# Performance work log

Measured on AMD Instinct MI355X. Metric: run time of the kernel, lower is better.

## Reference

```python
import jax, jax.numpy as jnp
import numpy as np

S, B, D, H, O = 128, 16, 512, 512, 256  # seq_len, batch, input=hidden (required equal), hidden, output

def setup_inputs() -> dict:
    key = jax.random.key(0)
    ks = jax.random.split(key, 11)
    sD = 1.0 / np.sqrt(D)
    sH = 1.0 / np.sqrt(H)
    g = lambda k, shape, s: (jax.random.normal(k, shape, dtype=jnp.float32) * s)
    return {
        "x": g(ks[0], (S, B, D), 1.0),
        # LocalAttention (undefined in source; feature-wise softmax gating): Linear(H,H)
        "attn_w": g(ks[1], (D, H), sD), "attn_b": g(ks[2], (H,), sD),
        "in_w": g(ks[3], (D, H), sD), "in_b": g(ks[4], (H,), sD),      # the_in
        "ins_w": g(ks[5], (H, H), sH), "ins_b": g(ks[6], (H,), sH),    # inside
        "sus_w": g(ks[7], (H, H), sH), "sus_b": g(ks[8], (H,), sH),    # suspend_state
        "out_w": g(ks[9], (H, O), sH), "out_b": g(ks[10], (O,), sH),   # output_layer
    }

def reference(x, attn_w, attn_b, in_w, in_b, ins_w, ins_b, sus_w, sus_b, out_w, out_b):
    S_, B_, _ = x.shape
    H_ = ins_w.shape[0]

    def step(carry, read):
        watch, sus = carry  # both [S,B,H] per the original broadcasting bug/behavior
        a = jax.nn.softmax(read @ attn_w + attn_b, axis=-1)  # [B,H]
        r = a * read                                          # [B,D]
        # [B,H] broadcasts over leading S dim of [S,B,H]
        watch = jnp.tanh((r @ in_w + in_b) + (watch @ ins_w + ins_b))
        sus = jnp.tanh((watch @ sus_w + sus_b) + sus)
        out = watch @ out_w + out_b                           # [S,B,O]
        return (watch, sus), out

    init = (jnp.zeros((S_, B_, H_), x.dtype), jnp.zeros((S_, B_, H_), x.dtype))
    (watch, sus), outs = jax.lax.scan(step, init, x)  # outs: [S,S,B,O]
    return outs, watch, sus
```

## Files before the change

kernel.cpp:

```cpp
#include <hip/hip_runtime.h>
#include <hip/hip_bf16.h>
#include <math.h>


#define S_LEN 128
#define B_SZ  16
#define H_SZ  512
#define O_SZ  256
#define ROWS  (S_LEN * B_SZ)

#define OUTS_ELEMS  (S_LEN * S_LEN * B_SZ * O_SZ)
#define WATCH_ELEMS (S_LEN * B_SZ * H_SZ)

typedef float  f32x4  __attribute__((ext_vector_type(4)));
typedef __bf16 bf16x8 __attribute__((ext_vector_type(8)));

struct alignas(16) GemmLds {
  __bf16 Ah[64][40]; __bf16 Al[64][40];
  __bf16 Bh[64][40]; __bf16 Bl[64][40];
};

__device__ __forceinline__ void gemm_body(
    const float* __restrict__ A, const float* __restrict__ B,
    const float* __restrict__ bias0, const float* __restrict__ bias1,
    float* __restrict__ C, int N, int K, int bm, int bn, GemmLds& T)
{
  const int tid = threadIdx.x;
  const int w = tid >> 6, l = tid & 63;
  const int fr = l & 15, fg = l >> 4;
  f32x4 acc[4] = {{0,0,0,0},{0,0,0,0},{0,0,0,0},{0,0,0,0}};
  const int ar = tid >> 2, ak = (tid & 3) << 3;
  const int bk = tid >> 3, bc = (tid & 7) << 3;

  for (int k0 = 0; k0 < K; k0 += 32) {
    {
      const float* s = &A[(size_t)(bm + ar) * K + k0 + ak];
      const f32x4 v0 = *(const f32x4*)s, v1 = *(const f32x4*)(s + 4);
      const float vv[8] = {v0.x, v0.y, v0.z, v0.w, v1.x, v1.y, v1.z, v1.w};
      bf16x8 h, lo;
#pragma unroll
      for (int j = 0; j < 8; ++j) {
        const __bf16 hh = (__bf16)vv[j];
        h[j] = hh; lo[j] = (__bf16)(vv[j] - (float)hh);
      }
      *(bf16x8*)&T.Ah[ar][ak] = h;
      *(bf16x8*)&T.Al[ar][ak] = lo;
    }
    {
      const float* s = &B[(size_t)(k0 + bk) * N + bn + bc];
      const f32x4 v0 = *(const f32x4*)s, v1 = *(const f32x4*)(s + 4);
      const float vv[8] = {v0.x, v0.y, v0.z, v0.w, v1.x, v1.y, v1.z, v1.w};
#pragma unroll
      for (int j = 0; j < 8; ++j) {
        const __bf16 hh = (__bf16)vv[j];
        T.Bh[bc + j][bk] = hh;
        T.Bl[bc + j][bk] = (__bf16)(vv[j] - (float)hh);
      }
    }
    __syncthreads();
    const bf16x8 ah = *(const bf16x8*)&T.Ah[(w << 4) + fr][fg << 3];
    const bf16x8 al = *(const bf16x8*)&T.Al[(w << 4) + fr][fg << 3];
#pragma unroll
    for (int nr = 0; nr < 4; ++nr) {
      const bf16x8 bh = *(const bf16x8*)&T.Bh[(nr << 4) + fr][fg << 3];
      const bf16x8 bl = *(const bf16x8*)&T.Bl[(nr << 4) + fr][fg << 3];
      acc[nr] = __builtin_amdgcn_mfma_f32_16x16x32_bf16(ah, bh, acc[nr], 0, 0, 0);
      acc[nr] = __builtin_amdgcn_mfma_f32_16x16x32_bf16(al, bh, acc[nr], 0, 0, 0);
      acc[nr] = __builtin_amdgcn_mfma_f32_16x16x32_bf16(ah, bl, acc[nr], 0, 0, 0);
    }
    __syncthreads();
  }
#pragma unroll
  for (int nr = 0; nr < 4; ++nr) {
    const int gcol = bn + (nr << 4) + fr;
    float bb = bias0 ? bias0[gcol] : 0.f;
    if (bias1) bb += bias1[gcol];
#pragma unroll
    for (int r = 0; r < 4; ++r) {
      const int grow = bm + (w << 4) + (fg << 2) + r;
      C[(size_t)grow * N + gcol] = acc[nr][r] + bb;
    }
  }
}

__global__ __launch_bounds__(256) void gemm_mfma(
    const float* __restrict__ A, const float* __restrict__ B,
    const float* __restrict__ bias0, const float* __restrict__ bias1,
    float* __restrict__ C, int N, int K)
{
  __shared__ GemmLds T;
  gemm_body(A, B, bias0, bias1, C, N, K, blockIdx.y << 6, blockIdx.x << 6, T);
}

__global__ __launch_bounds__(256) void gemm_dual_mfma(
    const float* __restrict__ A,
    const float* __restrict__ B1, const float* __restrict__ b1, float* __restrict__ C1,
    const float* __restrict__ B2, const float* __restrict__ b2, float* __restrict__ C2)
{
  __shared__ GemmLds T;
  if (blockIdx.x < 8)
    gemm_body(A, B1, b1, nullptr, C1, 512, 512, blockIdx.y << 6, blockIdx.x << 6, T);
  else
    gemm_body(A, B2, b2, nullptr, C2, 256, 512, blockIdx.y << 6, (blockIdx.x - 8) << 6, T);
}

__global__ __launch_bounds__(64) void softmax_gate(float* __restrict__ lg,
                                                   const float* __restrict__ x)
{
  const int r = blockIdx.x;
  const int lane = threadIdx.x;
  float v[8];
  float m = -1e30f;
#pragma unroll
  for (int i = 0; i < 8; ++i) {
    v[i] = lg[(r << 9) + (i << 6) + lane];
    m = fmaxf(m, v[i]);
  }
#pragma unroll
  for (int off = 32; off > 0; off >>= 1) m = fmaxf(m, __shfl_xor(m, off, 64));
  float s = 0.f;
#pragma unroll
  for (int i = 0; i < 8; ++i) { v[i] = expf(v[i] - m); s += v[i]; }
#pragma unroll
  for (int off = 32; off > 0; off >>= 1) s += __shfl_xor(s, off, 64);
  const float inv = 1.0f / s;
#pragma unroll
  for (int i = 0; i < 8; ++i) {
    const int idx = (r << 9) + (i << 6) + lane;
    lg[idx] = v[i] * inv * x[idx];
  }
}

__global__ __launch_bounds__(256, 1) void recurrence(
    const float* __restrict__ cbuf,
    const float* __restrict__ insw,
    float* __restrict__ wall,
    unsigned long long* __restrict__ pz)
{
  __shared__ float wsm[H_SZ];
  __shared__ float red[4][64];
  __shared__ int okf[4];

  const int wg  = blockIdx.x;
  const int b   = wg & 15;
  const int p   = wg >> 4;
  const int tid = threadIdx.x;
  const int cl  = tid & 63;
  const int kq  = tid >> 6;
  const int c   = (p << 6) + cl;
  const int kbase = kq << 7;

  f32x4 wr[32];
#pragma unroll
  for (int j = 0; j < 32; ++j) {
    wr[j].x = insw[((kbase + 4 * j + 0) << 9) + c];
    wr[j].y = insw[((kbase + 4 * j + 1) << 9) + c];
    wr[j].z = insw[((kbase + 4 * j + 2) << 9) + c];
    wr[j].w = insw[((kbase + 4 * j + 3) << 9) + c];
  }

  if (tid < 64) {
    const float v = tanhf(cbuf[(b << 9) + c]);
    wall[(b << 9) + c] = v;
    const unsigned long long pk =
        (1ULL << 32) | (unsigned long long)__float_as_uint(v);
    __hip_atomic_store(&pz[(b << 9) + c], pk, __ATOMIC_RELAXED,
                       __HIP_MEMORY_SCOPE_AGENT);
  }

  for (int t = 1; t < S_LEN; ++t) {
    const float cv = cbuf[(t << 13) + (b << 9) + c];

    const unsigned long long* src =
        pz + (((t - 1) & 15) << 13) + (b << 9);
    unsigned long long v0, v1;
    for (;;) {
      v0 = __hip_atomic_load(&src[2 * tid], __ATOMIC_RELAXED,
                             __HIP_MEMORY_SCOPE_AGENT);
      v1 = __hip_atomic_load(&src[2 * tid + 1], __ATOMIC_RELAXED,
                             __HIP_MEMORY_SCOPE_AGENT);
      const bool ok = ((unsigned)(v0 >> 32) == (unsigned)t) &
                      ((unsigned)(v1 >> 32) == (unsigned)t);
      const unsigned long long m = __ballot(ok);
      if ((tid & 63) == 0) okf[tid >> 6] = (m + 1 == 0ULL);
      __syncthreads();
      const bool all = okf[0] && okf[1] && okf[2] && okf[3];
      __syncthreads();
      if (all) break;
    }
    wsm[2 * tid]     = __uint_as_float((unsigned)v0);
    wsm[2 * tid + 1] = __uint_as_float((unsigned)v1);
    __syncthreads();

    float a0 = 0.f, a1 = 0.f, a2 = 0.f, a3 = 0.f;
#pragma unroll
    for (int j = 0; j < 32; ++j) {
      const f32x4 wv = *(const f32x4*)&wsm[kbase + (j << 2)];
      a0 = fmaf(wr[j].x, wv.x, a0);
      a1 = fmaf(wr[j].y, wv.y, a1);
      a2 = fmaf(wr[j].z, wv.z, a2);
      a3 = fmaf(wr[j].w, wv.w, a3);
    }
    red[kq][cl] = (a0 + a1) + (a2 + a3);
    __syncthreads();
    if (tid < 64) {
      const float y = red[0][cl] + red[1][cl] + red[2][cl] + red[3][cl];
      const float v = tanhf(cv + y);
      wall[(t << 13) + (b << 9) + c] = v;
      const unsigned long long pk =
          ((unsigned long long)(unsigned)(t + 1) << 32) |
          (unsigned long long)__float_as_uint(v);
      __hip_atomic_store(&pz[((t & 15) << 13) + (b << 9) + c], pk,
                         __ATOMIC_RELAXED, __HIP_MEMORY_SCOPE_AGENT);
    }
  }
}

__global__ __launch_bounds__(256) void sus_scan(
    const float* __restrict__ M, float* __restrict__ s_small)
{
  const int gid = blockIdx.x * blockDim.x + threadIdx.x;
  float s = 0.f;
  float n0 = M[gid];
  float n1 = M[(1 << 13) + gid];
  float n2 = M[(2 << 13) + gid];
  float n3 = M[(3 << 13) + gid];
  for (int t = 0; t < S_LEN - 4; ++t) {
    const float cur = n0;
    n0 = n1; n1 = n2; n2 = n3;
    n3 = M[((t + 4) << 13) + gid];
    s = tanhf(cur + s);
  }
  s = tanhf(n0 + s); s = tanhf(n1 + s); s = tanhf(n2 + s); s = tanhf(n3 + s);
  s_small[gid] = s;
}

__global__ __launch_bounds__(256) void finalize(
    const f32x4* __restrict__ os4, f32x4* __restrict__ outs4,
    const f32x4* __restrict__ w127, const f32x4* __restrict__ s4,
    f32x4* __restrict__ watch_out, f32x4* __restrict__ sus_out)
{
  const int gid = blockIdx.x * blockDim.x + threadIdx.x;
  const int stride = gridDim.x * blockDim.x;
  for (int i = gid; i < (1 << 24); i += stride) {
    const int o4 = i & 63;
    const int b  = (i >> 6) & 15;
    const int t  = i >> 17;
    __builtin_nontemporal_store(os4[(((t << 4) + b) << 6) + o4], &outs4[i]);
  }
  if (gid < (1 << 18)) {
    const int src = gid & 2047;
    __builtin_nontemporal_store(w127[src], &watch_out[gid]);
    __builtin_nontemporal_store(s4[src], &sus_out[gid]);
  }
}

extern "C" void kernel_launch(void* const* d_in, const int* in_sizes, int n_in,
                              void* d_out, int out_size, void* d_ws, size_t ws_size,
                              hipStream_t stream)
{
  const float* x      = (const float*)d_in[0];
  const float* attn_w = (const float*)d_in[1];
  const float* attn_b = (const float*)d_in[2];
  const float* in_w   = (const float*)d_in[3];
  const float* in_b   = (const float*)d_in[4];
  const float* ins_w  = (const float*)d_in[5];
  const float* ins_b  = (const float*)d_in[6];
  const float* sus_w  = (const float*)d_in[7];
  const float* sus_b  = (const float*)d_in[8];
  const float* out_w  = (const float*)d_in[9];
  const float* out_b  = (const float*)d_in[10];

  float* ws    = (float*)d_ws;
  float* cbuf  = ws;
  float* wallb = ws + (1 << 20);
  float* tmp   = ws + (2 << 20);
  float* mbuf  = tmp;
  unsigned long long* pz = (unsigned long long*)(ws + (3 << 20));
  float* obuf    = ws;
  float* s_small = ws + (1 << 19);

  float* outp   = (float*)d_out;
  float* watchp = outp + OUTS_ELEMS;
  float* susp   = watchp + WATCH_ELEMS;

  const dim3 blk(256);
  gemm_mfma<<<dim3(8, 32), blk, 0, stream>>>(x, attn_w, attn_b, nullptr, tmp, 512, 512);
  softmax_gate<<<dim3(2048), dim3(64), 0, stream>>>(tmp, x);
  gemm_mfma<<<dim3(8, 32), blk, 0, stream>>>(tmp, in_w, in_b, ins_b, cbuf, 512, 512);
  recurrence<<<dim3(128), blk, 0, stream>>>(cbuf, ins_w, wallb, pz);
  gemm_dual_mfma<<<dim3(12, 32), blk, 0, stream>>>(wallb, sus_w, sus_b, mbuf,
                                                   out_w, out_b, obuf);
  sus_scan<<<dim3(32), blk, 0, stream>>>(mbuf, s_small);
  finalize<<<dim3(4096), blk, 0, stream>>>(
      (const f32x4*)obuf, (f32x4*)d_out,
      (const f32x4*)(wallb + (127 << 13)), (const f32x4*)s_small,
      (f32x4*)watchp, (f32x4*)susp);
}
```

Before: 385.5 us.

## Remap recurrence blocks so each batch stays on one XCD and poll through L2

Workgroups of the recurrence kernel are remapped so that all eight column-slice blocks of a batch land on the same XCD, given round-robin XCD dispatch. Each step's state is also written to a second flag buffer that is polled with sc0 loads, which hit the XCD-local L2, with a fallback agent-scope atomic load every fourth iteration. The spin loop's double barrier is replaced by double-buffered ok flags, leaving one __syncthreads per poll. The aim is lower inter-block handoff latency per time step, at the cost of relying on the XCD placement assumption and on the visibility semantics of the volatile stores and sc0 loads.

```diff
diff --git a/kernel.cpp b/kernel.cpp
--- a/kernel.cpp
+++ b/kernel.cpp
@@ -135,15 +135,18 @@
     const float* __restrict__ cbuf,
     const float* __restrict__ insw,
     float* __restrict__ wall,
-    unsigned long long* __restrict__ pz)
+    unsigned long long* __restrict__ pz,
+    unsigned long long* __restrict__ pzf)
 {
   __shared__ float wsm[H_SZ];
   __shared__ float red[4][64];
-  __shared__ int okf[4];
+  __shared__ int okf[2][4];
 
   const int wg  = blockIdx.x;
-  const int b   = wg & 15;
-  const int p   = wg >> 4;
+  const int xcd = wg & 7;
+  const int idx = wg >> 3;
+  const int b   = xcd + ((idx & 8) ? 8 : 0);
+  const int p   = idx & 7;
   const int tid = threadIdx.x;
   const int cl  = tid & 63;
   const int kq  = tid >> 6;
@@ -164,6 +167,7 @@
     wall[(b << 9) + c] = v;
     const unsigned long long pk =
         (1ULL << 32) | (unsigned long long)__float_as_uint(v);
+    *(volatile unsigned long long*)&pzf[(b << 9) + c] = pk;
     __hip_atomic_store(&pz[(b << 9) + c], pk, __ATOMIC_RELAXED,
                        __HIP_MEMORY_SCOPE_AGENT);
   }
@@ -171,22 +175,34 @@
   for (int t = 1; t < S_LEN; ++t) {
     const float cv = cbuf[(t << 13) + (b << 9) + c];
 
-    const unsigned long long* src =
-        pz + (((t - 1) & 15) << 13) + (b << 9);
+    const unsigned long long* fsrc = pzf + (((t - 1) & 15) << 13) + (b << 9);
+    const unsigned long long* src  = pz  + (((t - 1) & 15) << 13) + (b << 9);
     unsigned long long v0, v1;
-    for (;;) {
-      v0 = __hip_atomic_load(&src[2 * tid], __ATOMIC_RELAXED,
-                             __HIP_MEMORY_SCOPE_AGENT);
-      v1 = __hip_atomic_load(&src[2 * tid + 1], __ATOMIC_RELAXED,
-                             __HIP_MEMORY_SCOPE_AGENT);
-      const bool ok = ((unsigned)(v0 >> 32) == (unsigned)t) &
-                      ((unsigned)(v1 >> 32) == (unsigned)t);
+    for (int it = 0;; ++it) {
+      unsigned long long a0, a1;
+      if ((it & 3) == 3) {
+        a0 = __hip_atomic_load(&src[2 * tid], __ATOMIC_RELAXED,
+                               __HIP_MEMORY_SCOPE_AGENT);
+        a1 = __hip_atomic_load(&src[2 * tid + 1], __ATOMIC_RELAXED,
+                               __HIP_MEMORY_SCOPE_AGENT);
+      } else {
+        const unsigned long long* p0 = &fsrc[2 * tid];
+        asm volatile(
+            "global_load_dwordx2 %0, %2, off sc0\n"
+            "global_load_dwordx2 %1, %2, off offset:8 sc0\n"
+            "s_waitcnt vmcnt(0)"
+            : "=&v"(a0), "=&v"(a1)
+            : "v"(p0));
+      }
+      const bool ok = ((unsigned)(a0 >> 32) == (unsigned)t) &
+                      ((unsigned)(a1 >> 32) == (unsigned)t);
       const unsigned long long m = __ballot(ok);
-      if ((tid & 63) == 0) okf[tid >> 6] = (m + 1 == 0ULL);
+      if ((tid & 63) == 0) okf[it & 1][tid >> 6] = (m + 1 == 0ULL);
       __syncthreads();
-      const bool all = okf[0] && okf[1] && okf[2] && okf[3];
-      __syncthreads();
-      if (all) break;
+      if (okf[it & 1][0] && okf[it & 1][1] && okf[it & 1][2] && okf[it & 1][3]) {
+        v0 = a0; v1 = a1;
+        break;
+      }
     }
     wsm[2 * tid]     = __uint_as_float((unsigned)v0);
     wsm[2 * tid + 1] = __uint_as_float((unsigned)v1);
@@ -210,6 +226,7 @@
       const unsigned long long pk =
           ((unsigned long long)(unsigned)(t + 1) << 32) |
           (unsigned long long)__float_as_uint(v);
+      *(volatile unsigned long long*)&pzf[((t & 15) << 13) + (b << 9) + c] = pk;
       __hip_atomic_store(&pz[((t & 15) << 13) + (b << 9) + c], pk,
                          __ATOMIC_RELAXED, __HIP_MEMORY_SCOPE_AGENT);
     }
@@ -276,7 +293,10 @@
   float* wallb = ws + (1 << 20);
   float* tmp   = ws + (2 << 20);
   float* mbuf  = tmp;
-  unsigned long long* pz = (unsigned long long*)(ws + (3 << 20));
+  unsigned long long* pz  = (unsigned long long*)(ws + (3 << 20));
+  unsigned long long* pzf = (ws_size >= ((size_t)14 << 20))
+      ? (unsigned long long*)(ws + (3 << 20) + (1 << 18))
+      : pz;
   float* obuf    = ws;
   float* s_small = ws + (1 << 19);
 
@@ -288,7 +308,7 @@
   gemm_mfma<<<dim3(8, 32), blk, 0, stream>>>(x, attn_w, attn_b, nullptr, tmp, 512, 512);
   softmax_gate<<<dim3(2048), dim3(64), 0, stream>>>(tmp, x);
   gemm_mfma<<<dim3(8, 32), blk, 0, stream>>>(tmp, in_w, in_b, ins_b, cbuf, 512, 512);
-  recurrence<<<dim3(128), blk, 0, stream>>>(cbuf, ins_w, wallb, pz);
+  recurrence<<<dim3(128), blk, 0, stream>>>(cbuf, ins_w, wallb, pz, pzf);
   gemm_dual_mfma<<<dim3(12, 32), blk, 0, stream>>>(wallb, sus_w, sus_b, mbuf,
                                                    out_w, out_b, obuf);
   sus_scan<<<dim3(32), blk, 0, stream>>>(mbuf, s_small);
```

New measurement: 519.8 us. 34.8% more time.

## Fuse recurrence with per-step output and suspend GEMMs via flag-polling consumer blocks

Applied to the files above, without the earlier changes.

The recurrence kernel now launches 128 extra consumer blocks, one per timestep. Each waits on a flagged copy of that step's watch values, then computes the out and sus projections with split-bf16 MFMA. The out rows are written straight into the 128-fold broadcast output, so output writes and GEMMs overlap the serial recurrence and the separate dual-GEMM and full finalize copy go away. The cost is a memset for the flags and 24-bit truncation of watch values fed to the projections, which lowers precision. It also assumes all 256 blocks are co-resident so the spin waits cannot deadlock.

```diff
diff --git a/kernel.cpp b/kernel.cpp
--- a/kernel.cpp
+++ b/kernel.cpp
@@ -92,18 +92,6 @@
   gemm_body(A, B, bias0, bias1, C, N, K, blockIdx.y << 6, blockIdx.x << 6, T);
 }
 
-__global__ __launch_bounds__(256) void gemm_dual_mfma(
-    const float* __restrict__ A,
-    const float* __restrict__ B1, const float* __restrict__ b1, float* __restrict__ C1,
-    const float* __restrict__ B2, const float* __restrict__ b2, float* __restrict__ C2)
-{
-  __shared__ GemmLds T;
-  if (blockIdx.x < 8)
-    gemm_body(A, B1, b1, nullptr, C1, 512, 512, blockIdx.y << 6, blockIdx.x << 6, T);
-  else
-    gemm_body(A, B2, b2, nullptr, C2, 256, 512, blockIdx.y << 6, (blockIdx.x - 8) << 6, T);
-}
-
 __global__ __launch_bounds__(64) void softmax_gate(float* __restrict__ lg,
                                                    const float* __restrict__ x)
 {
@@ -131,87 +119,236 @@
   }
 }
 
-__global__ __launch_bounds__(256, 1) void recurrence(
+#define RAW_BYTES 90624
+
+__global__ __launch_bounds__(256, 1) void rec_fused(
     const float* __restrict__ cbuf,
     const float* __restrict__ insw,
-    float* __restrict__ wall,
-    unsigned long long* __restrict__ pz)
-{
-  __shared__ float wsm[H_SZ];
-  __shared__ float red[4][64];
-  __shared__ int okf[4];
-
+    const float* __restrict__ outw,
+    const float* __restrict__ outb,
+    const float* __restrict__ susw,
+    const float* __restrict__ susb,
+    unsigned long long* __restrict__ pz,
+    unsigned* __restrict__ pzw,
+    float* __restrict__ w127g,
+    float* __restrict__ mbuf,
+    float* __restrict__ outp)
+{
+  __shared__ __align__(16) char raw[RAW_BYTES];
   const int wg  = blockIdx.x;
-  const int b   = wg & 15;
-  const int p   = wg >> 4;
   const int tid = threadIdx.x;
-  const int cl  = tid & 63;
-  const int kq  = tid >> 6;
-  const int c   = (p << 6) + cl;
-  const int kbase = kq << 7;
-
-  f32x4 wr[32];
-#pragma unroll
-  for (int j = 0; j < 32; ++j) {
-    wr[j].x = insw[((kbase + 4 * j + 0) << 9) + c];
-    wr[j].y = insw[((kbase + 4 * j + 1) << 9) + c];
-    wr[j].z = insw[((kbase + 4 * j + 2) << 9) + c];
-    wr[j].w = insw[((kbase + 4 * j + 3) << 9) + c];
-  }
-
-  if (tid < 64) {
-    const float v = tanhf(cbuf[(b << 9) + c]);
-    wall[(b << 9) + c] = v;
-    const unsigned long long pk =
-        (1ULL << 32) | (unsigned long long)__float_as_uint(v);
-    __hip_atomic_store(&pz[(b << 9) + c], pk, __ATOMIC_RELAXED,
-                       __HIP_MEMORY_SCOPE_AGENT);
-  }
-
-  for (int t = 1; t < S_LEN; ++t) {
-    const float cv = cbuf[(t << 13) + (b << 9) + c];
-
-    const unsigned long long* src =
-        pz + (((t - 1) & 15) << 13) + (b << 9);
-    unsigned long long v0, v1;
-    for (;;) {
-      v0 = __hip_atomic_load(&src[2 * tid], __ATOMIC_RELAXED,
-                             __HIP_MEMORY_SCOPE_AGENT);
-      v1 = __hip_atomic_load(&src[2 * tid + 1], __ATOMIC_RELAXED,
-                             __HIP_MEMORY_SCOPE_AGENT);
-      const bool ok = ((unsigned)(v0 >> 32) == (unsigned)t) &
-                      ((unsigned)(v1 >> 32) == (unsigned)t);
-      const unsigned long long m = __ballot(ok);
-      if ((tid & 63) == 0) okf[tid >> 6] = (m + 1 == 0ULL);
+
+  if (wg < 128) {
+    float* wsm = (float*)raw;
+    float (*red)[64] = (float (*)[64])(raw + 2048);
+    int* okf = (int*)(raw + 3072);
+
+    const int b   = wg & 15;
+    const int p   = wg >> 4;
+    const int cl  = tid & 63;
+    const int kq  = tid >> 6;
+    const int c   = (p << 6) + cl;
+    const int kbase = kq << 7;
+
+    f32x4 wr[32];
+#pragma unroll
+    for (int j = 0; j < 32; ++j) {
+      wr[j].x = insw[((kbase + 4 * j + 0) << 9) + c];
+      wr[j].y = insw[((kbase + 4 * j + 1) << 9) + c];
+      wr[j].z = insw[((kbase + 4 * j + 2) << 9) + c];
+      wr[j].w = insw[((kbase + 4 * j + 3) << 9) + c];
+    }
+
+    if (tid < 64) {
+      const float v = tanhf(cbuf[(b << 9) + c]);
+      const unsigned bits = __float_as_uint(v);
+      const unsigned long long pk =
+          (1ULL << 32) | (unsigned long long)bits;
+      __hip_atomic_store(&pz[(b << 9) + c], pk, __ATOMIC_RELAXED,
+                         __HIP_MEMORY_SCOPE_AGENT);
+      __hip_atomic_store(&pzw[(b << 9) + c], (1u << 24) | (bits >> 8),
+                         __ATOMIC_RELAXED, __HIP_MEMORY_SCOPE_AGENT);
+    }
+
+    for (int t = 1; t < S_LEN; ++t) {
+      const float cv = cbuf[(t << 13) + (b << 9) + c];
+
+      const unsigned long long* src =
+          pz + (((t - 1) & 15) << 13) + (b << 9);
+      unsigned long long v0, v1;
+      for (;;) {
+        v0 = __hip_atomic_load(&src[2 * tid], __ATOMIC_RELAXED,
+                               __HIP_MEMORY_SCOPE_AGENT);
+        v1 = __hip_atomic_load(&src[2 * tid + 1], __ATOMIC_RELAXED,
+                               __HIP_MEMORY_SCOPE_AGENT);
+        const bool ok = ((unsigned)(v0 >> 32) == (unsigned)t) &
+                        ((unsigned)(v1 >> 32) == (unsigned)t);
+        const unsigned long long m = __ballot(ok);
+        if ((tid & 63) == 0) okf[tid >> 6] = (m + 1 == 0ULL);
+        __syncthreads();
+        const bool all = okf[0] && okf[1] && okf[2] && okf[3];
+        __syncthreads();
+        if (all) break;
+      }
+      wsm[2 * tid]     = __uint_as_float((unsigned)v0);
+      wsm[2 * tid + 1] = __uint_as_float((unsigned)v1);
       __syncthreads();
-      const bool all = okf[0] && okf[1] && okf[2] && okf[3];
+
+      float a0 = 0.f, a1 = 0.f, a2 = 0.f, a3 = 0.f;
+#pragma unroll
+      for (int j = 0; j < 32; ++j) {
+        const f32x4 wv = *(const f32x4*)&wsm[kbase + (j << 2)];
+        a0 = fmaf(wr[j].x, wv.x, a0);
+        a1 = fmaf(wr[j].y, wv.y, a1);
+        a2 = fmaf(wr[j].z, wv.z, a2);
+        a3 = fmaf(wr[j].w, wv.w, a3);
+      }
+      red[kq][cl] = (a0 + a1) + (a2 + a3);
       __syncthreads();
-      if (all) break;
-    }
-    wsm[2 * tid]     = __uint_as_float((unsigned)v0);
-    wsm[2 * tid + 1] = __uint_as_float((unsigned)v1);
-    __syncthreads();
-
-    float a0 = 0.f, a1 = 0.f, a2 = 0.f, a3 = 0.f;
-#pragma unroll
-    for (int j = 0; j < 32; ++j) {
-      const f32x4 wv = *(const f32x4*)&wsm[kbase + (j << 2)];
-      a0 = fmaf(wr[j].x, wv.x, a0);
-      a1 = fmaf(wr[j].y, wv.y, a1);
-      a2 = fmaf(wr[j].z, wv.z, a2);
-      a3 = fmaf(wr[j].w, wv.w, a3);
-    }
-    red[kq][cl] = (a0 + a1) + (a2 + a3);
-    __syncthreads();
-    if (tid < 64) {
-      const float y = red[0][cl] + red[1][cl] + red[2][cl] + red[3][cl];
-      const float v = tanhf(cv + y);
-      wall[(t << 13) + (b << 9) + c] = v;
-      const unsigned long long pk =
-          ((unsigned long long)(unsigned)(t + 1) << 32) |
-          (unsigned long long)__float_as_uint(v);
-      __hip_atomic_store(&pz[((t & 15) << 13) + (b << 9) + c], pk,
-                         __ATOMIC_RELAXED, __HIP_MEMORY_SCOPE_AGENT);
+      if (tid < 64) {
+        const float y = red[0][cl] + red[1][cl] + red[2][cl] + red[3][cl];
+        const float v = tanhf(cv + y);
+        const unsigned bits = __float_as_uint(v);
+        const unsigned long long pk =
+            ((unsigned long long)(unsigned)(t + 1) << 32) |
+            (unsigned long long)bits;
+        __hip_atomic_store(&pz[((t & 15) << 13) + (b << 9) + c], pk,
+                           __ATOMIC_RELAXED, __HIP_MEMORY_SCOPE_AGENT);
+        __hip_atomic_store(&pzw[(t << 13) + (b << 9) + c],
+                           (((unsigned)(t + 1)) << 24) | (bits >> 8),
+                           __ATOMIC_RELAXED, __HIP_MEMORY_SCOPE_AGENT);
+        if (t == 127) w127g[(b << 9) + c] = v;
+      }
+    }
+  } else {
+    const int t  = wg - 128;
+    const int l  = tid & 63, q = tid >> 6;
+    const int fr = l & 15, fg = l >> 4;
+    float*  wtile = (float*)raw;
+    __bf16* Bh    = (__bf16*)(raw + 33280);
+    __bf16* Bl    = (__bf16*)(raw + 53760);
+    float*  osbuf = (float*)(raw + 74240);
+
+    {
+      const unsigned* src = pzw + (t << 13);
+      const unsigned tg = (unsigned)(t + 1);
+      for (int g = 0; g < 4; ++g) {
+        unsigned v[8];
+        int cnt = 0;
+        for (;;) {
+          bool ok = true;
+#pragma unroll
+          for (int i = 0; i < 8; ++i) {
+            v[i] = __hip_atomic_load(&src[(g << 11) + (i << 8) + tid],
+                                     __ATOMIC_RELAXED, __HIP_MEMORY_SCOPE_AGENT);
+            ok &= ((v[i] >> 24) == tg);
+          }
+          if (__ballot(ok) == ~0ULL) break;
+          if (cnt < 4)      __builtin_amdgcn_s_sleep(8);
+          else if (cnt < 8) __builtin_amdgcn_s_sleep(32);
+          else              __builtin_amdgcn_s_sleep(120);
+          ++cnt;
+        }
+#pragma unroll
+        for (int i = 0; i < 8; ++i) {
+          const int idx = (g << 11) + (i << 8) + tid;
+          wtile[(idx >> 9) * 520 + (idx & 511)] = __uint_as_float(v[i] << 8);
+        }
+      }
+      __syncthreads();
+    }
+
+    {
+      f32x4 acc[4] = {{0,0,0,0},{0,0,0,0},{0,0,0,0},{0,0,0,0}};
+      for (int k0 = 0; k0 < 512; k0 += 32) {
+#pragma unroll
+        for (int kk = 0; kk < 32; ++kk) {
+          const float v = outw[((k0 + kk) << 8) + tid];
+          const __bf16 h = (__bf16)v;
+          Bh[tid * 40 + kk] = h;
+          Bl[tid * 40 + kk] = (__bf16)(v - (float)h);
+        }
+        __syncthreads();
+        bf16x8 ah, al;
+#pragma unroll
+        for (int j = 0; j < 8; ++j) {
+          const float v = wtile[fr * 520 + k0 + (fg << 3) + j];
+          const __bf16 h = (__bf16)v;
+          ah[j] = h; al[j] = (__bf16)(v - (float)h);
+        }
+#pragma unroll
+        for (int nr = 0; nr < 4; ++nr) {
+          const int col = (q << 6) + (nr << 4) + fr;
+          const bf16x8 bh = *(const bf16x8*)&Bh[col * 40 + (fg << 3)];
+          const bf16x8 bl = *(const bf16x8*)&Bl[col * 40 + (fg << 3)];
+          acc[nr] = __builtin_amdgcn_mfma_f32_16x16x32_bf16(ah, bh, acc[nr], 0, 0, 0);
+          acc[nr] = __builtin_amdgcn_mfma_f32_16x16x32_bf16(al, bh, acc[nr], 0, 0, 0);
+          acc[nr] = __builtin_amdgcn_mfma_f32_16x16x32_bf16(ah, bl, acc[nr], 0, 0, 0);
+        }
+        __syncthreads();
+      }
+#pragma unroll
+      for (int nr = 0; nr < 4; ++nr) {
+        const int col = (q << 6) + (nr << 4) + fr;
+#pragma unroll
+        for (int r = 0; r < 4; ++r)
+          osbuf[((fg << 2) + r) * 256 + col] = acc[nr][r] + outb[col];
+      }
+      __syncthreads();
+    }
+
+    {
+      const int rb = tid >> 4, o0 = (tid & 15) << 4;
+      const f32x4 d0 = *(const f32x4*)&osbuf[rb * 256 + o0];
+      const f32x4 d1 = *(const f32x4*)&osbuf[rb * 256 + o0 + 4];
+      const f32x4 d2 = *(const f32x4*)&osbuf[rb * 256 + o0 + 8];
+      const f32x4 d3 = *(const f32x4*)&osbuf[rb * 256 + o0 + 12];
+      f32x4* dst = (f32x4*)(outp + (size_t)t * 524288) + (tid << 2);
+      for (int s = 0; s < S_LEN; ++s) {
+        __builtin_nontemporal_store(d0, dst + 0);
+        __builtin_nontemporal_store(d1, dst + 1);
+        __builtin_nontemporal_store(d2, dst + 2);
+        __builtin_nontemporal_store(d3, dst + 3);
+        dst += 1024;
+      }
+    }
+
+    for (int half = 0; half < 2; ++half) {
+      f32x4 am[4] = {{0,0,0,0},{0,0,0,0},{0,0,0,0},{0,0,0,0}};
+      for (int k0 = 0; k0 < 512; k0 += 32) {
+#pragma unroll
+        for (int kk = 0; kk < 32; ++kk) {
+          const float v = susw[((k0 + kk) << 9) + (half << 8) + tid];
+          const __bf16 h = (__bf16)v;
+          Bh[tid * 40 + kk] = h;
+          Bl[tid * 40 + kk] = (__bf16)(v - (float)h);
+        }
+        __syncthreads();
+        bf16x8 ah, al;
+#pragma unroll
+        for (int j = 0; j < 8; ++j) {
+          const float v = wtile[fr * 520 + k0 + (fg << 3) + j];
+          const __bf16 h = (__bf16)v;
+          ah[j] = h; al[j] = (__bf16)(v - (float)h);
+        }
+#pragma unroll
+        for (int nr = 0; nr < 4; ++nr) {
+          const int col = (q << 6) + (nr << 4) + fr;
+          const bf16x8 bh = *(const bf16x8*)&Bh[col * 40 + (fg << 3)];
+          const bf16x8 bl = *(const bf16x8*)&Bl[col * 40 + (fg << 3)];
+          am[nr] = __builtin_amdgcn_mfma_f32_16x16x32_bf16(ah, bh, am[nr], 0, 0, 0);
+          am[nr] = __builtin_amdgcn_mfma_f32_16x16x32_bf16(al, bh, am[nr], 0, 0, 0);
+          am[nr] = __builtin_amdgcn_mfma_f32_16x16x32_bf16(ah, bl, am[nr], 0, 0, 0);
+        }
+        __syncthreads();
+      }
+#pragma unroll
+      for (int nr = 0; nr < 4; ++nr) {
+        const int col = (half << 8) + (q << 6) + (nr << 4) + fr;
+#pragma unroll
+        for (int r = 0; r < 4; ++r)
+          mbuf[(t << 13) + (((fg << 2) + r) << 9) + col] = am[nr][r] + susb[col];
+      }
     }
   }
 }
@@ -235,23 +372,15 @@
   s_small[gid] = s;
 }
 
-__global__ __launch_bounds__(256) void finalize(
-    const f32x4* __restrict__ os4, f32x4* __restrict__ outs4,
+__global__ __launch_bounds__(256) void bc_watch_sus(
     const f32x4* __restrict__ w127, const f32x4* __restrict__ s4,
     f32x4* __restrict__ watch_out, f32x4* __restrict__ sus_out)
 {
-  const int gid = blockIdx.x * blockDim.x + threadIdx.x;
   const int stride = gridDim.x * blockDim.x;
-  for (int i = gid; i < (1 << 24); i += stride) {
-    const int o4 = i & 63;
-    const int b  = (i >> 6) & 15;
-    const int t  = i >> 17;
-    __builtin_nontemporal_store(os4[(((t << 4) + b) << 6) + o4], &outs4[i]);
-  }
-  if (gid < (1 << 18)) {
-    const int src = gid & 2047;
-    __builtin_nontemporal_store(w127[src], &watch_out[gid]);
-    __builtin_nontemporal_store(s4[src], &sus_out[gid]);
+  for (int i = blockIdx.x * blockDim.x + threadIdx.x; i < (1 << 18); i += stride) {
+    const int src = i & 2047;
+    __builtin_nontemporal_store(w127[src], &watch_out[i]);
+    __builtin_nontemporal_store(s4[src], &sus_out[i]);
   }
 }
 
@@ -273,12 +402,12 @@
 
   float* ws    = (float*)d_ws;
   float* cbuf  = ws;
-  float* wallb = ws + (1 << 20);
-  float* tmp   = ws + (2 << 20);
-  float* mbuf  = tmp;
-  unsigned long long* pz = (unsigned long long*)(ws + (3 << 20));
-  float* obuf    = ws;
-  float* s_small = ws + (1 << 19);
+  float* tmp   = ws + (1 << 20);
+  unsigned* pzw = (unsigned*)tmp;
+  unsigned long long* pz = (unsigned long long*)(ws + (2 << 20));
+  float* mbuf   = ws + (((size_t)9 << 20) >> 2);
+  float* w127g  = ws + (((size_t)13 << 20) >> 2);
+  float* s_small = w127g + 8192;
 
   float* outp   = (float*)d_out;
   float* watchp = outp + OUTS_ELEMS;
@@ -288,12 +417,12 @@
   gemm_mfma<<<dim3(8, 32), blk, 0, stream>>>(x, attn_w, attn_b, nullptr, tmp, 512, 512);
   softmax_gate<<<dim3(2048), dim3(64), 0, stream>>>(tmp, x);
   gemm_mfma<<<dim3(8, 32), blk, 0, stream>>>(tmp, in_w, in_b, ins_b, cbuf, 512, 512);
-  recurrence<<<dim3(128), blk, 0, stream>>>(cbuf, ins_w, wallb, pz);
-  gemm_dual_mfma<<<dim3(12, 32), blk, 0, stream>>>(wallb, sus_w, sus_b, mbuf,
-                                                   out_w, out_b, obuf);
+  (void)hipMemsetAsync(pzw, 0, (size_t)4 << 20, stream);
+  rec_fused<<<dim3(256), blk, 0, stream>>>(cbuf, ins_w, out_w, out_b,
+                                           sus_w, sus_b, pz, pzw, w127g,
+                                           mbuf, outp);
   sus_scan<<<dim3(32), blk, 0, stream>>>(mbuf, s_small);
-  finalize<<<dim3(4096), blk, 0, stream>>>(
-      (const f32x4*)obuf, (f32x4*)d_out,
-      (const f32x4*)(wallb + (127 << 13)), (const f32x4*)s_small,
+  bc_watch_sus<<<dim3(512), blk, 0, stream>>>(
+      (const f32x4*)w127g, (const f32x4*)s_small,
       (f32x4*)watchp, (f32x4*)susp);
 }
```

New measurement: 445.7 us. 1.16x slower.
